# Optimization experiments

Hardware: AMD Instinct MI355X
Metric: run time of the kernel (lower is better)

Reference implementation:

```python
import jax, jax.numpy as jnp
import numpy as np

N_NODES = 50000
N_EDGES = 800000
N_GRAPHS = 64
F_IN, H1, H2, H3, N_CLS = 128, 512, 256, 128, 10
BN_EPS = 1e-5


def setup_inputs() -> dict:
    key = jax.random.key(0)
    ks = jax.random.split(key, 16)

    def lin(k, fi, fo):
        return jax.random.normal(k, (fi, fo), jnp.float32) / np.sqrt(fi).astype(np.float32)

    return {
        "x": jax.random.normal(ks[0], (N_NODES, F_IN), jnp.float32),
        "edge_index": jax.random.randint(ks[1], (2, N_EDGES), 0, N_NODES),
        "batch": jnp.sort(jax.random.randint(ks[2], (N_NODES,), 0, N_GRAPHS)),
        "W1": lin(ks[3], F_IN, H1), "b1": jnp.zeros((H1,), jnp.float32),
        "g1": jnp.ones((H1,), jnp.float32), "be1": jnp.zeros((H1,), jnp.float32),
        "W2": lin(ks[4], H1, H2), "b2": jnp.zeros((H2,), jnp.float32),
        "g2": jnp.ones((H2,), jnp.float32), "be2": jnp.zeros((H2,), jnp.float32),
        "W3": lin(ks[5], H2, H3), "b3": jnp.zeros((H3,), jnp.float32),
        "g3": jnp.ones((H3,), jnp.float32), "be3": jnp.zeros((H3,), jnp.float32),
        "Wo": lin(ks[6], H3, N_CLS), "bo": jnp.zeros((N_CLS,), jnp.float32),
    }


def _gcn_conv(x, row, col, W, b):
    # PyG GCNConv: h = x @ W; add self-loops; sym-normalized scatter-add; + bias
    n = x.shape[0]
    h = x @ W
    loop = jnp.arange(n, dtype=row.dtype)
    row2 = jnp.concatenate([row, loop])  # source nodes
    col2 = jnp.concatenate([col, loop])  # target nodes
    deg = jax.ops.segment_sum(jnp.ones_like(col2, dtype=h.dtype), col2, num_segments=n)
    dinv = jnp.where(deg > 0, jax.lax.rsqrt(deg), 0.0)
    norm = (dinv[row2] * dinv[col2])[:, None]
    agg = jax.ops.segment_sum(h[row2] * norm, col2, num_segments=n)
    return agg + b


def _bn(x, g, b):
    # training-mode BatchNorm over node dim (biased variance, eps=1e-5)
    mean = jnp.mean(x, axis=0)
    var = jnp.mean(jnp.square(x - mean), axis=0)
    return g * (x - mean) * jax.lax.rsqrt(var + BN_EPS) + b


def reference(x, edge_index, batch, W1, b1, g1, be1, W2, b2, g2, be2,
              W3, b3, g3, be3, Wo, bo):
    row, col = edge_index[0], edge_index[1]
    h = jax.nn.relu(_bn(_gcn_conv(x, row, col, W1, b1), g1, be1))
    h = jax.nn.relu(_bn(_gcn_conv(h, row, col, W2, b2), g2, be2))
    h = jax.nn.relu(_bn(_gcn_conv(h, row, col, W3, b3), g3, be3))
    # global_mean_pool over graph ids
    sums = jax.ops.segment_sum(h, batch, num_segments=N_GRAPHS)
    cnt = jax.ops.segment_sum(jnp.ones((h.shape[0],), h.dtype), batch, num_segments=N_GRAPHS)
    pooled = sums / jnp.maximum(cnt, 1.0)[:, None]
    return pooled @ Wo + bo
```

## Files before the change

### kernel.cpp

```cpp
#include <hip/hip_runtime.h>
#include <hip/hip_bf16.h>
#include <cstdint>
#include <cstddef>

#define NNODES 50000
#define NGRAPHS 64

typedef short bf16x8 __attribute__((ext_vector_type(8)));
typedef float f32x4 __attribute__((ext_vector_type(4)));

__device__ inline float bf2f(unsigned short u) {
    return __uint_as_float(((unsigned)u) << 16);
}
__device__ inline unsigned short f2bf(float f) {
    unsigned u = __float_as_uint(f);
    return (unsigned short)((u + 0x7fff + ((u >> 16) & 1)) >> 16);
}
__device__ inline void unpack8(uint4 u, float* v) {
    v[0] = bf2f((unsigned short)(u.x & 0xffff)); v[1] = bf2f((unsigned short)(u.x >> 16));
    v[2] = bf2f((unsigned short)(u.y & 0xffff)); v[3] = bf2f((unsigned short)(u.y >> 16));
    v[4] = bf2f((unsigned short)(u.z & 0xffff)); v[5] = bf2f((unsigned short)(u.z >> 16));
    v[6] = bf2f((unsigned short)(u.w & 0xffff)); v[7] = bf2f((unsigned short)(u.w >> 16));
}

__global__ void deg_count_k(const int* __restrict__ col, int* __restrict__ cnt, int ne) {
    int i = blockIdx.x * blockDim.x + threadIdx.x;
    if (i < ne) atomicAdd(&cnt[col[i]], 1);
}

__global__ __launch_bounds__(256) void scan1_k(const int* __restrict__ cnt, int* __restrict__ offs,
                                               int* __restrict__ bsum, float* __restrict__ dinv, int n) {
    int t = threadIdx.x;
    int base = blockIdx.x * 1024 + t * 4;
    int4 v = {0, 0, 0, 0};
    if (base + 3 < n) v = *reinterpret_cast<const int4*>(cnt + base);
    else {
        if (base + 0 < n) v.x = cnt[base + 0];
        if (base + 1 < n) v.y = cnt[base + 1];
        if (base + 2 < n) v.z = cnt[base + 2];
    }
    if (base + 0 < n) dinv[base + 0] = rsqrtf((float)(v.x + 1));
    if (base + 1 < n) dinv[base + 1] = rsqrtf((float)(v.y + 1));
    if (base + 2 < n) dinv[base + 2] = rsqrtf((float)(v.z + 1));
    if (base + 3 < n) dinv[base + 3] = rsqrtf((float)(v.w + 1));

    int s = v.x + v.y + v.z + v.w;
    __shared__ int lds[256];
    lds[t] = s;
    __syncthreads();
    #pragma unroll
    for (int d = 1; d < 256; d <<= 1) {
        int u = (t >= d) ? lds[t - d] : 0;
        __syncthreads();
        lds[t] += u;
        __syncthreads();
    }
    int excl = lds[t] - s;
    if (t == 255) bsum[blockIdx.x] = lds[t];

    if (base + 3 < n) {
        int4 o;
        o.x = excl; o.y = excl + v.x; o.z = o.y + v.y; o.w = o.z + v.z;
        *reinterpret_cast<int4*>(offs + base) = o;
    } else {
        int e = excl;
        if (base + 0 < n) { offs[base + 0] = e; e += v.x; }
        if (base + 1 < n) { offs[base + 1] = e; e += v.y; }
        if (base + 2 < n) { offs[base + 2] = e; }
    }
}

__global__ __launch_bounds__(256) void scan2_k(int* __restrict__ bsum, int nb) {
    __shared__ int lds[256];
    int t = threadIdx.x;
    int v = (t < nb) ? bsum[t] : 0;
    lds[t] = v;
    __syncthreads();
    #pragma unroll
    for (int d = 1; d < 256; d <<= 1) {
        int u = (t >= d) ? lds[t - d] : 0;
        __syncthreads();
        lds[t] += u;
        __syncthreads();
    }
    if (t < nb) bsum[t] = lds[t] - v;
}

__global__ __launch_bounds__(256) void scan3_k(int* __restrict__ offs, const int* __restrict__ bsum, int n) {
    int base = blockIdx.x * 1024 + threadIdx.x * 4;
    int add = bsum[blockIdx.x];
    if (base + 3 < n) {
        int4 o = *reinterpret_cast<int4*>(offs + base);
        o.x += add; o.y += add; o.z += add; o.w += add;
        *reinterpret_cast<int4*>(offs + base) = o;
    } else {
        for (int k = 0; k < 4; ++k)
            if (base + k < n) offs[base + k] += add;
    }
}

__global__ void scatter_k(const int* __restrict__ row_, const int* __restrict__ col_,
                          const int* __restrict__ offs, int* __restrict__ fill,
                          int* __restrict__ csr_row, int ne) {
    int e = blockIdx.x * blockDim.x + threadIdx.x;
    if (e >= ne) return;
    int r = row_[e], c = col_[e];
    int pos = offs[c] + atomicAdd(&fill[c], 1);
    csr_row[pos] = r;
}

__global__ void cvt_scale_k(const float* __restrict__ in, const float* __restrict__ dinv,
                            unsigned short* __restrict__ out, int n) {
    long long i = (long long)blockIdx.x * blockDim.x + threadIdx.x;
    long long total4 = (long long)n * 32;
    if (i >= total4) return;
    int r = (int)(i >> 5);
    float d = dinv[r];
    float4 v = reinterpret_cast<const float4*>(in)[i];
    uint2 o;
    o.x = (unsigned)f2bf(v.x * d) | ((unsigned)f2bf(v.y * d) << 16);
    o.y = (unsigned)f2bf(v.z * d) | ((unsigned)f2bf(v.w * d) << 16);
    reinterpret_cast<uint2*>(out)[i] = o;
}

__global__ void wtrans_all_k(const float* __restrict__ W1, const float* __restrict__ W2,
                             const float* __restrict__ W3,
                             unsigned short* __restrict__ Wt1, unsigned short* __restrict__ Wt2,
                             unsigned short* __restrict__ Wt3) {
    int idx = blockIdx.x * blockDim.x + threadIdx.x;
    if (idx < 65536) {
        int k = idx >> 9, m = idx & 511;
        Wt1[m * 128 + k] = f2bf(W1[idx]);
    } else if (idx < 196608) {
        int j = idx - 65536;
        int k = j >> 8, m = j & 255;
        Wt2[m * 512 + k] = f2bf(W2[j]);
    } else if (idx < 229376) {
        int j = idx - 196608;
        int k = j >> 7, m = j & 127;
        Wt3[m * 256 + k] = f2bf(W3[j]);
    }
}

template<int FC>
__global__ void agg_s_k(const unsigned short* __restrict__ in, const int* __restrict__ offs,
                        const int* __restrict__ cnt, const int* __restrict__ csr_row,
                        const float* __restrict__ dinv, unsigned short* __restrict__ out, int n) {
    constexpr int F   = 64 * FC;
    constexpr int LPE = (FC == 4) ? 32 : 16;
    constexpr int EPL = 64 / LPE;
    int node = blockIdx.x * 4 + (threadIdx.x >> 6);
    if (node >= n) return;
    int lane = threadIdx.x & 63;
    int sub = lane / LPE;
    int fl  = lane % LPE;
    const size_t foff = (size_t)fl * 8;

    float acc[8] = {};
    if (sub == 0) {
        uint4 u = *reinterpret_cast<const uint4*>(in + (size_t)node * F + foff);
        float v[8]; unpack8(u, v);
        #pragma unroll
        for (int i = 0; i < 8; ++i) acc[i] = v[i];
    }

    int s = offs[node], e1 = s + cnt[node];
    int eb = s;
    for (; eb + 2 * EPL <= e1; eb += 2 * EPL) {
        int r0 = csr_row[eb + sub];
        int r1 = csr_row[eb + EPL + sub];
        uint4 u0 = *reinterpret_cast<const uint4*>(in + (size_t)r0 * F + foff);
        uint4 u1 = *reinterpret_cast<const uint4*>(in + (size_t)r1 * F + foff);
        float v0[8], v1[8];
        unpack8(u0, v0); unpack8(u1, v1);
        #pragma unroll
        for (int i = 0; i < 8; ++i) acc[i] += v0[i] + v1[i];
    }
    for (; eb < e1; eb += EPL) {
        int e = eb + sub;
        bool ok = e < e1;
        int r = csr_row[ok ? e : e1 - 1];
        uint4 u = *reinterpret_cast<const uint4*>(in + (size_t)r * F + foff);
        float v[8]; unpack8(u, v);
        if (ok) {
            #pragma unroll
            for (int i = 0; i < 8; ++i) acc[i] += v[i];
        }
    }

    #pragma unroll
    for (int d = LPE; d < 64; d <<= 1) {
        #pragma unroll
        for (int i = 0; i < 8; ++i) acc[i] += __shfl_xor(acc[i], d, 64);
    }

    if (sub == 0) {
        float dn = dinv[node];
        uint4 o;
        o.x = (unsigned)f2bf(acc[0] * dn) | ((unsigned)f2bf(acc[1] * dn) << 16);
        o.y = (unsigned)f2bf(acc[2] * dn) | ((unsigned)f2bf(acc[3] * dn) << 16);
        o.z = (unsigned)f2bf(acc[4] * dn) | ((unsigned)f2bf(acc[5] * dn) << 16);
        o.w = (unsigned)f2bf(acc[6] * dn) | ((unsigned)f2bf(acc[7] * dn) << 16);
        *reinterpret_cast<uint4*>(out + (size_t)node * F + foff) = o;
    }
}

template<bool BN_A, bool SCALE_OUT, bool STATS>
__global__ __launch_bounds__(256) void gemm_bt_k(const unsigned short* __restrict__ A,
                                                 const unsigned short* __restrict__ B,
                                                 unsigned short* __restrict__ C,
                                                 const float* __restrict__ scale,
                                                 const float* __restrict__ shift,
                                                 const float* __restrict__ dinv,
                                                 float* __restrict__ sums,
                                                 float* __restrict__ sqs,
                                                 int n, int K, int M) {
    __shared__ unsigned short As[128][40];
    __shared__ unsigned short Bs[128][40];
    int tid = threadIdx.x;
    int wid = tid >> 6, lane = tid & 63;
    int wr = wid >> 1, wc = wid & 1;
    int row0 = blockIdx.y * 128, col0 = blockIdx.x * 128;

    f32x4 acc[4][4] = {};

    for (int kt = 0; kt < K; kt += 32) {
        int c8 = (tid & 3) * 8;
        float4 sc0, sc1, sh0, sh1;
        if (BN_A) {
            sc0 = *reinterpret_cast<const float4*>(scale + kt + c8);
            sc1 = *reinterpret_cast<const float4*>(scale + kt + c8 + 4);
            sh0 = *reinterpret_cast<const float4*>(shift + kt + c8);
            sh1 = *reinterpret_cast<const float4*>(shift + kt + c8 + 4);
        }
        #pragma unroll
        for (int h = 0; h < 2; ++h) {
            int r = (tid >> 2) + h * 64;
            int gr = row0 + r;
            bf16x8 va = {};
            if (gr < n) va = *reinterpret_cast<const bf16x8*>(A + (size_t)gr * K + kt + c8);
            if (BN_A) {
                #pragma unroll
                for (int t = 0; t < 8; ++t) {
                    float sct = (t < 4) ? (&sc0.x)[t] : (&sc1.x)[t - 4];
                    float sht = (t < 4) ? (&sh0.x)[t] : (&sh1.x)[t - 4];
                    float f = bf2f((unsigned short)va[t]);
                    va[t] = (short)f2bf(fmaxf(f * sct + sht, 0.f));
                }
            }
            *reinterpret_cast<bf16x8*>(&As[r][c8]) = va;
            bf16x8 vb = *reinterpret_cast<const bf16x8*>(B + (size_t)(col0 + r) * K + kt + c8);
            *reinterpret_cast<bf16x8*>(&Bs[r][c8]) = vb;
        }
        __syncthreads();

        bf16x8 af[4], bfr[4];
        int koff = (lane >> 4) * 8;
        #pragma unroll
        for (int f = 0; f < 4; ++f) {
            af[f]  = *reinterpret_cast<const bf16x8*>(&As[wr * 64 + f * 16 + (lane & 15)][koff]);
            bfr[f] = *reinterpret_cast<const bf16x8*>(&Bs[wc * 64 + f * 16 + (lane & 15)][koff]);
        }
        #pragma unroll
        for (int i = 0; i < 4; ++i)
            #pragma unroll
            for (int j = 0; j < 4; ++j)
                acc[i][j] = __builtin_amdgcn_mfma_f32_16x16x32_bf16(af[i], bfr[j], acc[i][j], 0, 0, 0);
        __syncthreads();
    }

    #pragma unroll
    for (int i = 0; i < 4; ++i) {
        #pragma unroll
        for (int q = 0; q < 4; ++q) {
            int gr = row0 + wr * 64 + i * 16 + (lane >> 4) * 4 + q;
            if (gr < n) {
                float dr = SCALE_OUT ? dinv[gr] : 1.0f;
                #pragma unroll
                for (int j = 0; j < 4; ++j) {
                    int gc = col0 + wc * 64 + j * 16 + (lane & 15);
                    C[(size_t)gr * M + gc] = f2bf(acc[i][j][q] * dr);
                }
            }
        }
    }

    if (STATS) {
        #pragma unroll
        for (int j = 0; j < 4; ++j) {
            float s = 0.f, q = 0.f;
            #pragma unroll
            for (int i = 0; i < 4; ++i)
                #pragma unroll
                for (int p = 0; p < 4; ++p) {
                    float v = acc[i][j][p];
                    s += v; q += v * v;
                }
            s += __shfl_xor(s, 16, 64); s += __shfl_xor(s, 32, 64);
            q += __shfl_xor(q, 16, 64); q += __shfl_xor(q, 32, 64);
            if ((lane >> 4) == 0) {
                int gc = col0 + wc * 64 + j * 16 + (lane & 15);
                atomicAdd(&sums[gc], s);
                atomicAdd(&sqs[gc], q);
            }
        }
    }
}

template<int F>
__global__ __launch_bounds__(256) void bn_stats_k(const unsigned short* __restrict__ in,
                                                  float* __restrict__ stat, int n) {
    constexpr int G   = F / 8;
    constexpr int RPP = 256 / G;
    int g  = threadIdx.x & (G - 1);
    int rl = threadIdx.x / G;

    float s[8] = {}, q[8] = {};
    for (int r = blockIdx.x * RPP + rl; r < n; r += gridDim.x * RPP) {
        uint4 u = *reinterpret_cast<const uint4*>(in + (size_t)r * F + g * 8);
        float v[8]; unpack8(u, v);
        #pragma unroll
        for (int i = 0; i < 8; ++i) { s[i] += v[i]; q[i] += v[i] * v[i]; }
    }

    __shared__ float lds[RPP][F];
    #pragma unroll
    for (int i = 0; i < 8; ++i) lds[rl][g * 8 + i] = s[i];
    __syncthreads();
    if (threadIdx.x < F) {
        float t = 0.f;
        #pragma unroll
        for (int rr = 0; rr < RPP; ++rr) t += lds[rr][threadIdx.x];
        atomicAdd(&stat[threadIdx.x], t);
    }
    __syncthreads();
    #pragma unroll
    for (int i = 0; i < 8; ++i) lds[rl][g * 8 + i] = q[i];
    __syncthreads();
    if (threadIdx.x < F) {
        float t = 0.f;
        #pragma unroll
        for (int rr = 0; rr < RPP; ++rr) t += lds[rr][threadIdx.x];
        atomicAdd(&stat[F + threadIdx.x], t);
    }
}

__global__ void bn_finalize_k(const float* __restrict__ stat,
                              const float* __restrict__ g, const float* __restrict__ be,
                              float* __restrict__ scale, float* __restrict__ shift,
                              int F, float invn) {
    int f = blockIdx.x * blockDim.x + threadIdx.x;
    if (f >= F) return;
    float mean = stat[f] * invn;
    float var  = stat[F + f] * invn - mean * mean;
    float rstd = rsqrtf(var + 1e-5f);
    float sc = g[f] * rstd;
    scale[f] = sc;
    shift[f] = be[f] - mean * sc;
}

__global__ void bounds_k(const int* __restrict__ batch, int* __restrict__ start, int n) {
    int i = blockIdx.x * blockDim.x + threadIdx.x;
    if (i >= n) return;
    int b = batch[i];
    if (i == 0) {
        for (int g = 0; g <= b; ++g) start[g] = 0;
    } else {
        int pb = batch[i - 1];
        for (int g = pb + 1; g <= b; ++g) start[g] = i;
    }
    if (i == n - 1) {
        for (int g = b + 1; g <= NGRAPHS; ++g) start[g] = n;
    }
}

__global__ __launch_bounds__(256) void pool_part_k(const unsigned short* __restrict__ a,
                                                   const int* __restrict__ start,
                                                   const float* __restrict__ scale,
                                                   const float* __restrict__ shift,
                                                   float* __restrict__ partial) {
    int g = blockIdx.x, q = blockIdx.y;
    int s = start[g], e = start[g + 1];
    int nr = e - s;
    int c0 = s + (nr * q) / 4, c1 = s + (nr * (q + 1)) / 4;
    int tf = threadIdx.x & 15, tr = threadIdx.x >> 4;

    float sc[8], sh[8];
    #pragma unroll
    for (int i = 0; i < 8; ++i) { sc[i] = scale[tf * 8 + i]; sh[i] = shift[tf * 8 + i]; }

    float acc[8] = {};
    for (int r = c0 + tr; r < c1; r += 16) {
        uint4 u = *reinterpret_cast<const uint4*>(a + (size_t)r * 128 + tf * 8);
        float v[8]; unpack8(u, v);
        #pragma unroll
        for (int i = 0; i < 8; ++i) acc[i] += fmaxf(v[i] * sc[i] + sh[i], 0.f);
    }

    __shared__ float red[16][128];
    #pragma unroll
    for (int i = 0; i < 8; ++i) red[tr][tf * 8 + i] = acc[i];
    __syncthreads();
    int f = threadIdx.x;
    if (f < 128) {
        float s2 = 0.f;
        #pragma unroll
        for (int t = 0; t < 16; ++t) s2 += red[t][f];
        partial[((size_t)(g * 4 + q)) * 128 + f] = s2;
    }
}

__global__ void final_out_k(const float* __restrict__ partial, const int* __restrict__ start,
                            const float* __restrict__ Wo, const float* __restrict__ bo,
                            float* __restrict__ out) {
    int idx = blockIdx.x * blockDim.x + threadIdx.x;
    if (idx >= NGRAPHS * 10) return;
    int g = idx / 10, c = idx - g * 10;
    float cntf = (float)(start[g + 1] - start[g]);
    float inv = 1.0f / fmaxf(cntf, 1.0f);
    float s = bo[c];
    for (int k = 0; k < 128; ++k) {
        float pk = partial[(size_t)(g * 4 + 0) * 128 + k] + partial[(size_t)(g * 4 + 1) * 128 + k]
                 + partial[(size_t)(g * 4 + 2) * 128 + k] + partial[(size_t)(g * 4 + 3) * 128 + k];
        s += pk * inv * Wo[k * 10 + c];
    }
    out[idx] = s;
}

extern "C" void kernel_launch(void* const* d_in, const int* in_sizes, int n_in,
                              void* d_out, int out_size, void* d_ws, size_t ws_size,
                              hipStream_t stream) {
    const float* x   = (const float*)d_in[0];
    const int*   ei  = (const int*)d_in[1];
    const int*   bat = (const int*)d_in[2];
    const float* W1  = (const float*)d_in[3];
    const float* g1  = (const float*)d_in[5];
    const float* be1 = (const float*)d_in[6];
    const float* W2  = (const float*)d_in[7];
    const float* g2  = (const float*)d_in[9];
    const float* be2 = (const float*)d_in[10];
    const float* W3  = (const float*)d_in[11];
    const float* g3  = (const float*)d_in[13];
    const float* be3 = (const float*)d_in[14];
    const float* Wo  = (const float*)d_in[15];
    const float* bo  = (const float*)d_in[16];
    float* out = (float*)d_out;

    const int n  = in_sizes[2];
    const int ne = in_sizes[1] / 2;
    const int* row = ei;
    const int* col = ei + ne;
    const int NB = (n + 1023) / 1024;

    char* base = (char*)d_ws;
    size_t o = 0;
    auto alloc = [&](size_t bytes) -> char* {
        char* p = base + o;
        o += (bytes + 255) & ~(size_t)255;
        return p;
    };
    int*   cntfill = (int*)alloc((size_t)2 * n * 4);
    int*   cnt  = cntfill;
    int*   fill = cntfill + n;
    float* statall = (float*)alloc((size_t)3 * 1024 * 4);
    float* stat1 = statall;
    float* stat2 = statall + 1024;
    float* stat3 = statall + 2048;
    size_t zspan = (size_t)((char*)(statall + 3 * 1024) - (char*)cntfill);

    int*   offs  = (int*)alloc(n * 4);
    int*   bsum  = (int*)alloc(256 * 4);
    float* dinv  = (float*)alloc(n * 4);
    int*   start = (int*)alloc((NGRAPHS + 1) * 4);
    float* scale = (float*)alloc(512 * 4);
    float* shift = (float*)alloc(512 * 4);
    float* partial = (float*)alloc((size_t)NGRAPHS * 4 * 128 * 4);
    int*   csr_row = (int*)alloc((size_t)ne * 4);
    unsigned short* Wt1 = (unsigned short*)alloc((size_t)128 * 512 * 2);
    unsigned short* Wt2 = (unsigned short*)alloc((size_t)512 * 256 * 2);
    unsigned short* Wt3 = (unsigned short*)alloc((size_t)256 * 128 * 2);
    unsigned short* xs_bf  = (unsigned short*)alloc((size_t)n * 128 * 2);
    unsigned short* ax_bf  = (unsigned short*)alloc((size_t)n * 128 * 2);
    unsigned short* h1_bf  = (unsigned short*)alloc((size_t)n * 512 * 2);
    unsigned short* t2s_bf = (unsigned short*)alloc((size_t)n * 256 * 2);
    unsigned short* a2_bf  = (unsigned short*)alloc((size_t)n * 256 * 2);
    unsigned short* t3s_bf = (unsigned short*)alloc((size_t)n * 128 * 2);
    unsigned short* a3_bf  = (unsigned short*)alloc((size_t)n * 128 * 2);

    hipMemsetAsync(cntfill, 0, zspan, stream);
    deg_count_k<<<(ne + 255) / 256, 256, 0, stream>>>(col, cnt, ne);
    scan1_k<<<NB, 256, 0, stream>>>(cnt, offs, bsum, dinv, n);
    scan2_k<<<1, 256, 0, stream>>>(bsum, NB);
    scan3_k<<<NB, 256, 0, stream>>>(offs, bsum, n);
    scatter_k<<<(ne + 255) / 256, 256, 0, stream>>>(row, col, offs, fill, csr_row, ne);
    bounds_k<<<(n + 255) / 256, 256, 0, stream>>>(bat, start, n);

    cvt_scale_k<<<(unsigned)(((long long)n * 32 + 255) / 256), 256, 0, stream>>>(x, dinv, xs_bf, n);
    wtrans_all_k<<<896, 256, 0, stream>>>(W1, W2, W3, Wt1, Wt2, Wt3);

    agg_s_k<2><<<(n + 3) / 4, 256, 0, stream>>>(xs_bf, offs, cnt, csr_row, dinv, ax_bf, n);
    gemm_bt_k<false, false, true><<<dim3(4, (n + 127) / 128), 256, 0, stream>>>(
        ax_bf, Wt1, h1_bf, nullptr, nullptr, nullptr, stat1, stat1 + 512, n, 128, 512);
    bn_finalize_k<<<2, 256, 0, stream>>>(stat1, g1, be1, scale, shift, 512, 1.0f / n);

    gemm_bt_k<true, true, false><<<dim3(2, (n + 127) / 128), 256, 0, stream>>>(
        h1_bf, Wt2, t2s_bf, scale, shift, dinv, nullptr, nullptr, n, 512, 256);
    agg_s_k<4><<<(n + 3) / 4, 256, 0, stream>>>(t2s_bf, offs, cnt, csr_row, dinv, a2_bf, n);
    bn_stats_k<256><<<1024, 256, 0, stream>>>(a2_bf, stat2, n);
    bn_finalize_k<<<1, 256, 0, stream>>>(stat2, g2, be2, scale, shift, 256, 1.0f / n);

    gemm_bt_k<true, true, false><<<dim3(1, (n + 127) / 128), 256, 0, stream>>>(
        a2_bf, Wt3, t3s_bf, scale, shift, dinv, nullptr, nullptr, n, 256, 128);
    agg_s_k<2><<<(n + 3) / 4, 256, 0, stream>>>(t3s_bf, offs, cnt, csr_row, dinv, a3_bf, n);
    bn_stats_k<128><<<1024, 256, 0, stream>>>(a3_bf, stat3, n);
    bn_finalize_k<<<1, 256, 0, stream>>>(stat3, g3, be3, scale, shift, 128, 1.0f / n);

    pool_part_k<<<dim3(NGRAPHS, 4), 256, 0, stream>>>(a3_bf, start, scale, shift, partial);
    final_out_k<<<3, 256, 0, stream>>>(partial, start, Wo, bo, out);
}
```

Before: 506.2 us.

## Fuse preprocessing, aggregation and tail stages into cooperative persistent kernels

Replaces about twenty small launches with three cooperative kernels that use grid-wide syncs: one for CSR build, conversion and the first aggregation, one for aggregation plus BN stats, and one for aggregation, stats, pooling and output. BN finalize is folded into the GEMM A-load and the pool kernel, so the separate finalize launches go away. The aim is to cut launch overhead and idle gaps between tiny kernels. In exchange, the grid-stride persistent loops can give lower parallelism or occupancy for the gather-heavy aggregation, and grid.sync adds its own cost. A non-cooperative fallback path is kept.

Measured after the change: 2.004 ms. 296% more time.

```diff
diff --git a/kernel.cpp b/kernel.cpp
--- a/kernel.cpp
+++ b/kernel.cpp
@@ -1,9 +1,11 @@
 #include <hip/hip_runtime.h>
 #include <hip/hip_bf16.h>
+#include <hip/hip_cooperative_groups.h>
 #include <cstdint>
 #include <cstddef>
 
-#define NNODES 50000
+namespace cg = cooperative_groups;
+
 #define NGRAPHS 64
 
 typedef short bf16x8 __attribute__((ext_vector_type(8)));
@@ -23,13 +25,10 @@
     v[6] = bf2f((unsigned short)(u.w & 0xffff)); v[7] = bf2f((unsigned short)(u.w >> 16));
 }
 
-__global__ void deg_count_k(const int* __restrict__ col, int* __restrict__ cnt, int ne) {
-    int i = blockIdx.x * blockDim.x + threadIdx.x;
-    if (i < ne) atomicAdd(&cnt[col[i]], 1);
-}
-
-__global__ __launch_bounds__(256) void scan1_k(const int* __restrict__ cnt, int* __restrict__ offs,
-                                               int* __restrict__ bsum, float* __restrict__ dinv, int n) {
+
+__device__ void scan1_body(const int* __restrict__ cnt, int* __restrict__ offs,
+                           int* __restrict__ bsum, float* __restrict__ dinv, int n) {
+    __shared__ int lds1[256];
     int t = threadIdx.x;
     int base = blockIdx.x * 1024 + t * 4;
     int4 v = {0, 0, 0, 0};
@@ -45,18 +44,17 @@
     if (base + 3 < n) dinv[base + 3] = rsqrtf((float)(v.w + 1));
 
     int s = v.x + v.y + v.z + v.w;
-    __shared__ int lds[256];
-    lds[t] = s;
+    lds1[t] = s;
     __syncthreads();
     #pragma unroll
     for (int d = 1; d < 256; d <<= 1) {
-        int u = (t >= d) ? lds[t - d] : 0;
-        __syncthreads();
-        lds[t] += u;
-        __syncthreads();
-    }
-    int excl = lds[t] - s;
-    if (t == 255) bsum[blockIdx.x] = lds[t];
+        int u = (t >= d) ? lds1[t - d] : 0;
+        __syncthreads();
+        lds1[t] += u;
+        __syncthreads();
+    }
+    int excl = lds1[t] - s;
+    if (t == 255) bsum[blockIdx.x] = lds1[t];
 
     if (base + 3 < n) {
         int4 o;
@@ -70,23 +68,23 @@
     }
 }
 
-__global__ __launch_bounds__(256) void scan2_k(int* __restrict__ bsum, int nb) {
-    __shared__ int lds[256];
+__device__ void scan2_body(int* __restrict__ bsum, int nb) {
+    __shared__ int lds2[256];
     int t = threadIdx.x;
     int v = (t < nb) ? bsum[t] : 0;
-    lds[t] = v;
+    lds2[t] = v;
     __syncthreads();
     #pragma unroll
     for (int d = 1; d < 256; d <<= 1) {
-        int u = (t >= d) ? lds[t - d] : 0;
-        __syncthreads();
-        lds[t] += u;
-        __syncthreads();
-    }
-    if (t < nb) bsum[t] = lds[t] - v;
-}
-
-__global__ __launch_bounds__(256) void scan3_k(int* __restrict__ offs, const int* __restrict__ bsum, int n) {
+        int u = (t >= d) ? lds2[t - d] : 0;
+        __syncthreads();
+        lds2[t] += u;
+        __syncthreads();
+    }
+    if (t < nb) bsum[t] = lds2[t] - v;
+}
+
+__device__ void scan3_body(int* __restrict__ offs, const int* __restrict__ bsum, int n) {
     int base = blockIdx.x * 1024 + threadIdx.x * 4;
     int add = bsum[blockIdx.x];
     if (base + 3 < n) {
@@ -99,21 +97,21 @@
     }
 }
 
-__global__ void scatter_k(const int* __restrict__ row_, const int* __restrict__ col_,
-                          const int* __restrict__ offs, int* __restrict__ fill,
-                          int* __restrict__ csr_row, int ne) {
-    int e = blockIdx.x * blockDim.x + threadIdx.x;
-    if (e >= ne) return;
-    int r = row_[e], c = col_[e];
-    int pos = offs[c] + atomicAdd(&fill[c], 1);
-    csr_row[pos] = r;
-}
-
-__global__ void cvt_scale_k(const float* __restrict__ in, const float* __restrict__ dinv,
-                            unsigned short* __restrict__ out, int n) {
-    long long i = (long long)blockIdx.x * blockDim.x + threadIdx.x;
-    long long total4 = (long long)n * 32;
-    if (i >= total4) return;
+__device__ inline void bounds_body(const int* __restrict__ batch, int* __restrict__ start, int i, int n) {
+    int b = batch[i];
+    if (i == 0) {
+        for (int g = 0; g <= b; ++g) start[g] = 0;
+    } else {
+        int pb = batch[i - 1];
+        for (int g = pb + 1; g <= b; ++g) start[g] = i;
+    }
+    if (i == n - 1) {
+        for (int g = b + 1; g <= NGRAPHS; ++g) start[g] = n;
+    }
+}
+
+__device__ inline void cvt_body(const float* __restrict__ in, const float* __restrict__ dinv,
+                                unsigned short* __restrict__ out, long long i) {
     int r = (int)(i >> 5);
     float d = dinv[r];
     float4 v = reinterpret_cast<const float4*>(in)[i];
@@ -123,11 +121,9 @@
     reinterpret_cast<uint2*>(out)[i] = o;
 }
 
-__global__ void wtrans_all_k(const float* __restrict__ W1, const float* __restrict__ W2,
-                             const float* __restrict__ W3,
-                             unsigned short* __restrict__ Wt1, unsigned short* __restrict__ Wt2,
-                             unsigned short* __restrict__ Wt3) {
-    int idx = blockIdx.x * blockDim.x + threadIdx.x;
+__device__ inline void wtrans_body(int idx, const float* __restrict__ W1, const float* __restrict__ W2,
+                                   const float* __restrict__ W3, unsigned short* __restrict__ Wt1,
+                                   unsigned short* __restrict__ Wt2, unsigned short* __restrict__ Wt3) {
     if (idx < 65536) {
         int k = idx >> 9, m = idx & 511;
         Wt1[m * 128 + k] = f2bf(W1[idx]);
@@ -135,7 +131,7 @@
         int j = idx - 65536;
         int k = j >> 8, m = j & 255;
         Wt2[m * 512 + k] = f2bf(W2[j]);
-    } else if (idx < 229376) {
+    } else {
         int j = idx - 196608;
         int k = j >> 7, m = j & 127;
         Wt3[m * 256 + k] = f2bf(W3[j]);
@@ -143,81 +139,271 @@
 }
 
 template<int FC>
-__global__ void agg_s_k(const unsigned short* __restrict__ in, const int* __restrict__ offs,
-                        const int* __restrict__ cnt, const int* __restrict__ csr_row,
-                        const float* __restrict__ dinv, unsigned short* __restrict__ out, int n) {
+__device__ void agg_body(const unsigned short* __restrict__ in, const int* __restrict__ offs,
+                         const int* __restrict__ cnt, const int* __restrict__ csr_row,
+                         const float* __restrict__ dinv, unsigned short* __restrict__ out, int n) {
     constexpr int F   = 64 * FC;
     constexpr int LPE = (FC == 4) ? 32 : 16;
     constexpr int EPL = 64 / LPE;
-    int node = blockIdx.x * 4 + (threadIdx.x >> 6);
-    if (node >= n) return;
+    int wave = threadIdx.x >> 6;
     int lane = threadIdx.x & 63;
     int sub = lane / LPE;
     int fl  = lane % LPE;
     const size_t foff = (size_t)fl * 8;
-
-    float acc[8] = {};
-    if (sub == 0) {
-        uint4 u = *reinterpret_cast<const uint4*>(in + (size_t)node * F + foff);
+    int ngrp = (n + 3) >> 2;
+
+    for (int grp = blockIdx.x; grp < ngrp; grp += gridDim.x) {
+        int node = grp * 4 + wave;
+        if (node >= n) continue;
+
+        float acc[8] = {};
+        if (sub == 0) {
+            uint4 u = *reinterpret_cast<const uint4*>(in + (size_t)node * F + foff);
+            float v[8]; unpack8(u, v);
+            #pragma unroll
+            for (int i = 0; i < 8; ++i) acc[i] = v[i];
+        }
+
+        int s = offs[node], e1 = s + cnt[node];
+        int eb = s;
+        for (; eb + 2 * EPL <= e1; eb += 2 * EPL) {
+            int r0 = csr_row[eb + sub];
+            int r1 = csr_row[eb + EPL + sub];
+            uint4 u0 = *reinterpret_cast<const uint4*>(in + (size_t)r0 * F + foff);
+            uint4 u1 = *reinterpret_cast<const uint4*>(in + (size_t)r1 * F + foff);
+            float v0[8], v1[8];
+            unpack8(u0, v0); unpack8(u1, v1);
+            #pragma unroll
+            for (int i = 0; i < 8; ++i) acc[i] += v0[i] + v1[i];
+        }
+        for (; eb < e1; eb += EPL) {
+            int e = eb + sub;
+            bool ok = e < e1;
+            int r = csr_row[ok ? e : e1 - 1];
+            uint4 u = *reinterpret_cast<const uint4*>(in + (size_t)r * F + foff);
+            float v[8]; unpack8(u, v);
+            if (ok) {
+                #pragma unroll
+                for (int i = 0; i < 8; ++i) acc[i] += v[i];
+            }
+        }
+
+        #pragma unroll
+        for (int d = LPE; d < 64; d <<= 1) {
+            #pragma unroll
+            for (int i = 0; i < 8; ++i) acc[i] += __shfl_xor(acc[i], d, 64);
+        }
+
+        if (sub == 0) {
+            float dn = dinv[node];
+            uint4 o;
+            o.x = (unsigned)f2bf(acc[0] * dn) | ((unsigned)f2bf(acc[1] * dn) << 16);
+            o.y = (unsigned)f2bf(acc[2] * dn) | ((unsigned)f2bf(acc[3] * dn) << 16);
+            o.z = (unsigned)f2bf(acc[4] * dn) | ((unsigned)f2bf(acc[5] * dn) << 16);
+            o.w = (unsigned)f2bf(acc[6] * dn) | ((unsigned)f2bf(acc[7] * dn) << 16);
+            *reinterpret_cast<uint4*>(out + (size_t)node * F + foff) = o;
+        }
+    }
+}
+
+template<int F>
+__device__ void bn_stats_body(const unsigned short* __restrict__ in, float* __restrict__ stat, int n) {
+    constexpr int G   = F / 8;
+    constexpr int RPP = 256 / G;
+    int g  = threadIdx.x & (G - 1);
+    int rl = threadIdx.x / G;
+
+    float s[8] = {}, q[8] = {};
+    for (int r = blockIdx.x * RPP + rl; r < n; r += gridDim.x * RPP) {
+        uint4 u = *reinterpret_cast<const uint4*>(in + (size_t)r * F + g * 8);
         float v[8]; unpack8(u, v);
         #pragma unroll
-        for (int i = 0; i < 8; ++i) acc[i] = v[i];
-    }
-
-    int s = offs[node], e1 = s + cnt[node];
-    int eb = s;
-    for (; eb + 2 * EPL <= e1; eb += 2 * EPL) {
-        int r0 = csr_row[eb + sub];
-        int r1 = csr_row[eb + EPL + sub];
-        uint4 u0 = *reinterpret_cast<const uint4*>(in + (size_t)r0 * F + foff);
-        uint4 u1 = *reinterpret_cast<const uint4*>(in + (size_t)r1 * F + foff);
-        float v0[8], v1[8];
-        unpack8(u0, v0); unpack8(u1, v1);
-        #pragma unroll
-        for (int i = 0; i < 8; ++i) acc[i] += v0[i] + v1[i];
-    }
-    for (; eb < e1; eb += EPL) {
-        int e = eb + sub;
-        bool ok = e < e1;
-        int r = csr_row[ok ? e : e1 - 1];
-        uint4 u = *reinterpret_cast<const uint4*>(in + (size_t)r * F + foff);
-        float v[8]; unpack8(u, v);
-        if (ok) {
+        for (int i = 0; i < 8; ++i) { s[i] += v[i]; q[i] += v[i] * v[i]; }
+    }
+
+    __shared__ float ldsb[RPP][F];
+    #pragma unroll
+    for (int i = 0; i < 8; ++i) ldsb[rl][g * 8 + i] = s[i];
+    __syncthreads();
+    if (threadIdx.x < F) {
+        float t = 0.f;
+        #pragma unroll
+        for (int rr = 0; rr < RPP; ++rr) t += ldsb[rr][threadIdx.x];
+        atomicAdd(&stat[threadIdx.x], t);
+    }
+    __syncthreads();
+    #pragma unroll
+    for (int i = 0; i < 8; ++i) ldsb[rl][g * 8 + i] = q[i];
+    __syncthreads();
+    if (threadIdx.x < F) {
+        float t = 0.f;
+        #pragma unroll
+        for (int rr = 0; rr < RPP; ++rr) t += ldsb[rr][threadIdx.x];
+        atomicAdd(&stat[F + threadIdx.x], t);
+    }
+}
+
+__device__ void pool_body(const unsigned short* __restrict__ a, const int* __restrict__ start,
+                          const float* __restrict__ stat3, const float* __restrict__ g3,
+                          const float* __restrict__ be3, float invn, float* __restrict__ partial) {
+    __shared__ float scp[128], shp[128];
+    __shared__ float red[16][128];
+    int tid = threadIdx.x;
+    if (tid < 128) {
+        float mean = stat3[tid] * invn;
+        float var  = stat3[128 + tid] * invn - mean * mean;
+        float sc = g3[tid] * rsqrtf(var + 1e-5f);
+        scp[tid] = sc;
+        shp[tid] = be3[tid] - mean * sc;
+    }
+    __syncthreads();
+    int tf = tid & 15, tr = tid >> 4;
+    float sc[8], sh[8];
+    #pragma unroll
+    for (int i = 0; i < 8; ++i) { sc[i] = scp[tf * 8 + i]; sh[i] = shp[tf * 8 + i]; }
+
+    for (int job = blockIdx.x; job < NGRAPHS * 4; job += gridDim.x) {
+        int g = job >> 2, q = job & 3;
+        int s = start[g], e = start[g + 1];
+        int nr = e - s;
+        int c0 = s + (nr * q) / 4, c1 = s + (nr * (q + 1)) / 4;
+
+        float acc[8] = {};
+        for (int r = c0 + tr; r < c1; r += 16) {
+            uint4 u = *reinterpret_cast<const uint4*>(a + (size_t)r * 128 + tf * 8);
+            float v[8]; unpack8(u, v);
             #pragma unroll
-            for (int i = 0; i < 8; ++i) acc[i] += v[i];
-        }
-    }
-
-    #pragma unroll
-    for (int d = LPE; d < 64; d <<= 1) {
-        #pragma unroll
-        for (int i = 0; i < 8; ++i) acc[i] += __shfl_xor(acc[i], d, 64);
-    }
-
-    if (sub == 0) {
-        float dn = dinv[node];
-        uint4 o;
-        o.x = (unsigned)f2bf(acc[0] * dn) | ((unsigned)f2bf(acc[1] * dn) << 16);
-        o.y = (unsigned)f2bf(acc[2] * dn) | ((unsigned)f2bf(acc[3] * dn) << 16);
-        o.z = (unsigned)f2bf(acc[4] * dn) | ((unsigned)f2bf(acc[5] * dn) << 16);
-        o.w = (unsigned)f2bf(acc[6] * dn) | ((unsigned)f2bf(acc[7] * dn) << 16);
-        *reinterpret_cast<uint4*>(out + (size_t)node * F + foff) = o;
-    }
-}
-
-template<bool BN_A, bool SCALE_OUT, bool STATS>
+            for (int i = 0; i < 8; ++i) acc[i] += fmaxf(v[i] * sc[i] + sh[i], 0.f);
+        }
+        #pragma unroll
+        for (int i = 0; i < 8; ++i) red[tr][tf * 8 + i] = acc[i];
+        __syncthreads();
+        if (tid < 128) {
+            float s2 = 0.f;
+            #pragma unroll
+            for (int t = 0; t < 16; ++t) s2 += red[t][tid];
+            partial[((size_t)job) * 128 + tid] = s2;
+        }
+        __syncthreads();
+    }
+}
+
+__device__ void final_body(const float* __restrict__ partial, const int* __restrict__ start,
+                           const float* __restrict__ Wo, const float* __restrict__ bo,
+                           float* __restrict__ out, int gtid, int gsz) {
+    for (int idx = gtid; idx < NGRAPHS * 10; idx += gsz) {
+        int g = idx / 10, c = idx - g * 10;
+        float cntf = (float)(start[g + 1] - start[g]);
+        float inv = 1.0f / fmaxf(cntf, 1.0f);
+        float s = bo[c];
+        for (int k = 0; k < 128; ++k) {
+            float pk = partial[(size_t)(g * 4 + 0) * 128 + k] + partial[(size_t)(g * 4 + 1) * 128 + k]
+                     + partial[(size_t)(g * 4 + 2) * 128 + k] + partial[(size_t)(g * 4 + 3) * 128 + k];
+            s += pk * inv * Wo[k * 10 + c];
+        }
+        out[idx] = s;
+    }
+}
+
+
+struct PrepArgs {
+    const float* x; const int* row; const int* col; const int* bat;
+    const float* W1; const float* W2; const float* W3;
+    int* cnt; int* fill; float* statall; int* offs; int* bsum; float* dinv; int* start;
+    int* csr_row;
+    unsigned short* Wt1; unsigned short* Wt2; unsigned short* Wt3;
+    unsigned short* xs; unsigned short* ax;
+    int n; int ne; int nb;
+};
+
+__global__ __launch_bounds__(256) void prep_coop_k(PrepArgs a) {
+    cg::grid_group grid = cg::this_grid();
+    int gsz  = gridDim.x * 256;
+    int gtid = blockIdx.x * 256 + threadIdx.x;
+
+    for (int i = gtid; i < a.n; i += gsz) { a.cnt[i] = 0; a.fill[i] = 0; }
+    for (int i = gtid; i < 3 * 1024; i += gsz) a.statall[i] = 0.f;
+    grid.sync();
+    for (int e = gtid; e < a.ne; e += gsz) atomicAdd(&a.cnt[a.col[e]], 1);
+    grid.sync();
+    if (blockIdx.x < a.nb) scan1_body(a.cnt, a.offs, a.bsum, a.dinv, a.n);
+    grid.sync();
+    if (blockIdx.x == 0) scan2_body(a.bsum, a.nb);
+    grid.sync();
+    if (blockIdx.x < a.nb) scan3_body(a.offs, a.bsum, a.n);
+    grid.sync();
+    for (int e = gtid; e < a.ne; e += gsz) {
+        int r = a.row[e], c = a.col[e];
+        int pos = a.offs[c] + atomicAdd(&a.fill[c], 1);
+        a.csr_row[pos] = r;
+    }
+    for (int i = gtid; i < a.n; i += gsz) bounds_body(a.bat, a.start, i, a.n);
+    long long total4 = (long long)a.n * 32;
+    for (long long i = gtid; i < total4; i += gsz) cvt_body(a.x, a.dinv, a.xs, i);
+    for (int i = gtid; i < 229376; i += gsz) wtrans_body(i, a.W1, a.W2, a.W3, a.Wt1, a.Wt2, a.Wt3);
+    grid.sync();
+    agg_body<2>(a.xs, a.offs, a.cnt, a.csr_row, a.dinv, a.ax, a.n);
+}
+
+struct MidArgs {
+    const unsigned short* t2s; const int* offs; const int* cnt; const int* csr_row;
+    const float* dinv; unsigned short* a2; float* stat2; int n;
+};
+
+__global__ __launch_bounds__(256) void mid_coop_k(MidArgs a) {
+    cg::grid_group grid = cg::this_grid();
+    agg_body<4>(a.t2s, a.offs, a.cnt, a.csr_row, a.dinv, a.a2, a.n);
+    grid.sync();
+    bn_stats_body<256>(a.a2, a.stat2, a.n);
+}
+
+struct TailArgs {
+    const unsigned short* t3s; const int* offs; const int* cnt; const int* csr_row;
+    const float* dinv; unsigned short* a3; float* stat3;
+    const float* g3; const float* be3; const int* start;
+    const float* Wo; const float* bo; float* partial; float* out; int n;
+};
+
+__global__ __launch_bounds__(256) void tail_coop_k(TailArgs a) {
+    cg::grid_group grid = cg::this_grid();
+    agg_body<2>(a.t3s, a.offs, a.cnt, a.csr_row, a.dinv, a.a3, a.n);
+    grid.sync();
+    bn_stats_body<128>(a.a3, a.stat3, a.n);
+    grid.sync();
+    pool_body(a.a3, a.start, a.stat3, a.g3, a.be3, 1.0f / a.n, a.partial);
+    grid.sync();
+    final_body(a.partial, a.start, a.Wo, a.bo, a.out, blockIdx.x * 256 + threadIdx.x, gridDim.x * 256);
+}
+
+template<bool BN_STAT, bool SCALE_OUT, bool STATS>
 __global__ __launch_bounds__(256) void gemm_bt_k(const unsigned short* __restrict__ A,
                                                  const unsigned short* __restrict__ B,
                                                  unsigned short* __restrict__ C,
-                                                 const float* __restrict__ scale,
-                                                 const float* __restrict__ shift,
+                                                 const float* __restrict__ stat_in,
+                                                 const float* __restrict__ gamma,
+                                                 const float* __restrict__ beta,
+                                                 float invn,
                                                  const float* __restrict__ dinv,
                                                  float* __restrict__ sums,
                                                  float* __restrict__ sqs,
                                                  int n, int K, int M) {
     __shared__ unsigned short As[128][40];
     __shared__ unsigned short Bs[128][40];
+    __shared__ float scs[BN_STAT ? 512 : 1];
+    __shared__ float shs[BN_STAT ? 512 : 1];
     int tid = threadIdx.x;
+
+    if (BN_STAT) {
+        for (int f = tid; f < K; f += 256) {
+            float mean = stat_in[f] * invn;
+            float var  = stat_in[K + f] * invn - mean * mean;
+            float sc = gamma[f] * rsqrtf(var + 1e-5f);
+            scs[f] = sc;
+            shs[f] = beta[f] - mean * sc;
+        }
+        __syncthreads();
+    }
+
     int wid = tid >> 6, lane = tid & 63;
     int wr = wid >> 1, wc = wid & 1;
     int row0 = blockIdx.y * 128, col0 = blockIdx.x * 128;
@@ -227,11 +413,11 @@
     for (int kt = 0; kt < K; kt += 32) {
         int c8 = (tid & 3) * 8;
         float4 sc0, sc1, sh0, sh1;
-        if (BN_A) {
-            sc0 = *reinterpret_cast<const float4*>(scale + kt + c8);
-            sc1 = *reinterpret_cast<const float4*>(scale + kt + c8 + 4);
-            sh0 = *reinterpret_cast<const float4*>(shift + kt + c8);
-            sh1 = *reinterpret_cast<const float4*>(shift + kt + c8 + 4);
+        if (BN_STAT) {
+            sc0 = *reinterpret_cast<const float4*>(&scs[kt + c8]);
+            sc1 = *reinterpret_cast<const float4*>(&scs[kt + c8 + 4]);
+            sh0 = *reinterpret_cast<const float4*>(&shs[kt + c8]);
+            sh1 = *reinterpret_cast<const float4*>(&shs[kt + c8 + 4]);
         }
         #pragma unroll
         for (int h = 0; h < 2; ++h) {
@@ -239,7 +425,7 @@
             int gr = row0 + r;
             bf16x8 va = {};
             if (gr < n) va = *reinterpret_cast<const bf16x8*>(A + (size_t)gr * K + kt + c8);
-            if (BN_A) {
+            if (BN_STAT) {
                 #pragma unroll
                 for (int t = 0; t < 8; ++t) {
                     float sct = (t < 4) ? (&sc0.x)[t] : (&sc1.x)[t - 4];
@@ -307,125 +493,58 @@
     }
 }
 
+
+__global__ void deg_count_k(const int* __restrict__ col, int* __restrict__ cnt, int ne) {
+    int i = blockIdx.x * blockDim.x + threadIdx.x;
+    if (i < ne) atomicAdd(&cnt[col[i]], 1);
+}
+__global__ __launch_bounds__(256) void scan1_k(const int* cnt, int* offs, int* bsum, float* dinv, int n) {
+    scan1_body(cnt, offs, bsum, dinv, n);
+}
+__global__ __launch_bounds__(256) void scan2_k(int* bsum, int nb) { scan2_body(bsum, nb); }
+__global__ __launch_bounds__(256) void scan3_k(int* offs, const int* bsum, int n) { scan3_body(offs, bsum, n); }
+
+__global__ void prep3_k(const int* __restrict__ row_, const int* __restrict__ col_,
+                        const int* __restrict__ offs, int* __restrict__ fill, int* __restrict__ csr_row,
+                        const int* __restrict__ bat, int* __restrict__ start,
+                        const float* __restrict__ x, const float* __restrict__ dinv,
+                        unsigned short* __restrict__ xs,
+                        const float* __restrict__ W1, const float* __restrict__ W2, const float* __restrict__ W3,
+                        unsigned short* __restrict__ Wt1, unsigned short* __restrict__ Wt2,
+                        unsigned short* __restrict__ Wt3, int n, int ne) {
+    int gsz  = gridDim.x * blockDim.x;
+    int gtid = blockIdx.x * blockDim.x + threadIdx.x;
+    for (int e = gtid; e < ne; e += gsz) {
+        int r = row_[e], c = col_[e];
+        int pos = offs[c] + atomicAdd(&fill[c], 1);
+        csr_row[pos] = r;
+    }
+    for (int i = gtid; i < n; i += gsz) bounds_body(bat, start, i, n);
+    long long total4 = (long long)n * 32;
+    for (long long i = gtid; i < total4; i += gsz) cvt_body(x, dinv, xs, i);
+    for (int i = gtid; i < 229376; i += gsz) wtrans_body(i, W1, W2, W3, Wt1, Wt2, Wt3);
+}
+
+template<int FC>
+__global__ void agg_k(const unsigned short* in, const int* offs, const int* cnt, const int* csr_row,
+                      const float* dinv, unsigned short* out, int n) {
+    agg_body<FC>(in, offs, cnt, csr_row, dinv, out, n);
+}
 template<int F>
-__global__ __launch_bounds__(256) void bn_stats_k(const unsigned short* __restrict__ in,
-                                                  float* __restrict__ stat, int n) {
-    constexpr int G   = F / 8;
-    constexpr int RPP = 256 / G;
-    int g  = threadIdx.x & (G - 1);
-    int rl = threadIdx.x / G;
-
-    float s[8] = {}, q[8] = {};
-    for (int r = blockIdx.x * RPP + rl; r < n; r += gridDim.x * RPP) {
-        uint4 u = *reinterpret_cast<const uint4*>(in + (size_t)r * F + g * 8);
-        float v[8]; unpack8(u, v);
-        #pragma unroll
-        for (int i = 0; i < 8; ++i) { s[i] += v[i]; q[i] += v[i] * v[i]; }
-    }
-
-    __shared__ float lds[RPP][F];
-    #pragma unroll
-    for (int i = 0; i < 8; ++i) lds[rl][g * 8 + i] = s[i];
-    __syncthreads();
-    if (threadIdx.x < F) {
-        float t = 0.f;
-        #pragma unroll
-        for (int rr = 0; rr < RPP; ++rr) t += lds[rr][threadIdx.x];
-        atomicAdd(&stat[threadIdx.x], t);
-    }
-    __syncthreads();
-    #pragma unroll
-    for (int i = 0; i < 8; ++i) lds[rl][g * 8 + i] = q[i];
-    __syncthreads();
-    if (threadIdx.x < F) {
-        float t = 0.f;
-        #pragma unroll
-        for (int rr = 0; rr < RPP; ++rr) t += lds[rr][threadIdx.x];
-        atomicAdd(&stat[F + threadIdx.x], t);
-    }
-}
-
-__global__ void bn_finalize_k(const float* __restrict__ stat,
-                              const float* __restrict__ g, const float* __restrict__ be,
-                              float* __restrict__ scale, float* __restrict__ shift,
-                              int F, float invn) {
-    int f = blockIdx.x * blockDim.x + threadIdx.x;
-    if (f >= F) return;
-    float mean = stat[f] * invn;
-    float var  = stat[F + f] * invn - mean * mean;
-    float rstd = rsqrtf(var + 1e-5f);
-    float sc = g[f] * rstd;
-    scale[f] = sc;
-    shift[f] = be[f] - mean * sc;
-}
-
-__global__ void bounds_k(const int* __restrict__ batch, int* __restrict__ start, int n) {
-    int i = blockIdx.x * blockDim.x + threadIdx.x;
-    if (i >= n) return;
-    int b = batch[i];
-    if (i == 0) {
-        for (int g = 0; g <= b; ++g) start[g] = 0;
-    } else {
-        int pb = batch[i - 1];
-        for (int g = pb + 1; g <= b; ++g) start[g] = i;
-    }
-    if (i == n - 1) {
-        for (int g = b + 1; g <= NGRAPHS; ++g) start[g] = n;
-    }
-}
-
-__global__ __launch_bounds__(256) void pool_part_k(const unsigned short* __restrict__ a,
-                                                   const int* __restrict__ start,
-                                                   const float* __restrict__ scale,
-                                                   const float* __restrict__ shift,
-                                                   float* __restrict__ partial) {
-    int g = blockIdx.x, q = blockIdx.y;
-    int s = start[g], e = start[g + 1];
-    int nr = e - s;
-    int c0 = s + (nr * q) / 4, c1 = s + (nr * (q + 1)) / 4;
-    int tf = threadIdx.x & 15, tr = threadIdx.x >> 4;
-
-    float sc[8], sh[8];
-    #pragma unroll
-    for (int i = 0; i < 8; ++i) { sc[i] = scale[tf * 8 + i]; sh[i] = shift[tf * 8 + i]; }
-
-    float acc[8] = {};
-    for (int r = c0 + tr; r < c1; r += 16) {
-        uint4 u = *reinterpret_cast<const uint4*>(a + (size_t)r * 128 + tf * 8);
-        float v[8]; unpack8(u, v);
-        #pragma unroll
-        for (int i = 0; i < 8; ++i) acc[i] += fmaxf(v[i] * sc[i] + sh[i], 0.f);
-    }
-
-    __shared__ float red[16][128];
-    #pragma unroll
-    for (int i = 0; i < 8; ++i) red[tr][tf * 8 + i] = acc[i];
-    __syncthreads();
-    int f = threadIdx.x;
-    if (f < 128) {
-        float s2 = 0.f;
-        #pragma unroll
-        for (int t = 0; t < 16; ++t) s2 += red[t][f];
-        partial[((size_t)(g * 4 + q)) * 128 + f] = s2;
-    }
-}
-
-__global__ void final_out_k(const float* __restrict__ partial, const int* __restrict__ start,
-                            const float* __restrict__ Wo, const float* __restrict__ bo,
-                            float* __restrict__ out) {
-    int idx = blockIdx.x * blockDim.x + threadIdx.x;
-    if (idx >= NGRAPHS * 10) return;
-    int g = idx / 10, c = idx - g * 10;
-    float cntf = (float)(start[g + 1] - start[g]);
-    float inv = 1.0f / fmaxf(cntf, 1.0f);
-    float s = bo[c];
-    for (int k = 0; k < 128; ++k) {
-        float pk = partial[(size_t)(g * 4 + 0) * 128 + k] + partial[(size_t)(g * 4 + 1) * 128 + k]
-                 + partial[(size_t)(g * 4 + 2) * 128 + k] + partial[(size_t)(g * 4 + 3) * 128 + k];
-        s += pk * inv * Wo[k * 10 + c];
-    }
-    out[idx] = s;
-}
+__global__ __launch_bounds__(256) void bn_stats_k(const unsigned short* in, float* stat, int n) {
+    bn_stats_body<F>(in, stat, n);
+}
+__global__ __launch_bounds__(256) void pool_k(const unsigned short* a, const int* start,
+                                              const float* stat3, const float* g3, const float* be3,
+                                              float invn, float* partial) {
+    pool_body(a, start, stat3, g3, be3, invn, partial);
+}
+__global__ void final_out_k(const float* partial, const int* start, const float* Wo,
+                            const float* bo, float* out) {
+    final_body(partial, start, Wo, bo, out, blockIdx.x * blockDim.x + threadIdx.x,
+               gridDim.x * blockDim.x);
+}
+
 
 extern "C" void kernel_launch(void* const* d_in, const int* in_sizes, int n_in,
                               void* d_out, int out_size, void* d_ws, size_t ws_size,
@@ -466,14 +585,11 @@
     float* stat1 = statall;
     float* stat2 = statall + 1024;
     float* stat3 = statall + 2048;
-    size_t zspan = (size_t)((char*)(statall + 3 * 1024) - (char*)cntfill);
 
     int*   offs  = (int*)alloc(n * 4);
     int*   bsum  = (int*)alloc(256 * 4);
     float* dinv  = (float*)alloc(n * 4);
     int*   start = (int*)alloc((NGRAPHS + 1) * 4);
-    float* scale = (float*)alloc(512 * 4);
-    float* shift = (float*)alloc(512 * 4);
     float* partial = (float*)alloc((size_t)NGRAPHS * 4 * 128 * 4);
     int*   csr_row = (int*)alloc((size_t)ne * 4);
     unsigned short* Wt1 = (unsigned short*)alloc((size_t)128 * 512 * 2);
@@ -487,34 +603,72 @@
     unsigned short* t3s_bf = (unsigned short*)alloc((size_t)n * 128 * 2);
     unsigned short* a3_bf  = (unsigned short*)alloc((size_t)n * 128 * 2);
 
-    hipMemsetAsync(cntfill, 0, zspan, stream);
-    deg_count_k<<<(ne + 255) / 256, 256, 0, stream>>>(col, cnt, ne);
-    scan1_k<<<NB, 256, 0, stream>>>(cnt, offs, bsum, dinv, n);
-    scan2_k<<<1, 256, 0, stream>>>(bsum, NB);
-    scan3_k<<<NB, 256, 0, stream>>>(offs, bsum, n);
-    scatter_k<<<(ne + 255) / 256, 256, 0, stream>>>(row, col, offs, fill, csr_row, ne);
-    bounds_k<<<(n + 255) / 256, 256, 0, stream>>>(bat, start, n);
-
-    cvt_scale_k<<<(unsigned)(((long long)n * 32 + 255) / 256), 256, 0, stream>>>(x, dinv, xs_bf, n);
-    wtrans_all_k<<<896, 256, 0, stream>>>(W1, W2, W3, Wt1, Wt2, Wt3);
-
-    agg_s_k<2><<<(n + 3) / 4, 256, 0, stream>>>(xs_bf, offs, cnt, csr_row, dinv, ax_bf, n);
+    const float invn = 1.0f / (float)n;
+
+    PrepArgs pa = { x, row, col, bat, W1, W2, W3, cnt, fill, statall, offs, bsum, dinv, start,
+                    csr_row, Wt1, Wt2, Wt3, xs_bf, ax_bf, n, ne, NB };
+    MidArgs  ma = { t2s_bf, offs, cnt, csr_row, dinv, a2_bf, stat2, n };
+    TailArgs ta = { t3s_bf, offs, cnt, csr_row, dinv, a3_bf, stat3, g3, be3, start,
+                    Wo, bo, partial, out, n };
+
+    bool coop = true;
+    {
+        int occ = 0;
+        if (hipOccupancyMaxActiveBlocksPerMultiprocessor(&occ, prep_coop_k, 256, 0) != hipSuccess || occ < 1)
+            occ = 2;
+        int G = occ * 256; if (G > 4096) G = 4096;
+        void* args[] = { &pa };
+        hipError_t e = hipLaunchCooperativeKernel((const void*)prep_coop_k, dim3(G), dim3(256), args, 0, stream);
+        if (e != hipSuccess) { coop = false; (void)hipGetLastError(); }
+    }
+    if (!coop) {
+        hipMemsetAsync(cntfill, 0, (size_t)2 * n * 4, stream);
+        hipMemsetAsync(statall, 0, 3 * 1024 * 4, stream);
+        deg_count_k<<<(ne + 255) / 256, 256, 0, stream>>>(col, cnt, ne);
+        scan1_k<<<NB, 256, 0, stream>>>(cnt, offs, bsum, dinv, n);
+        scan2_k<<<1, 256, 0, stream>>>(bsum, NB);
+        scan3_k<<<NB, 256, 0, stream>>>(offs, bsum, n);
+        prep3_k<<<2048, 256, 0, stream>>>(row, col, offs, fill, csr_row, bat, start,
+                                          x, dinv, xs_bf, W1, W2, W3, Wt1, Wt2, Wt3, n, ne);
+        agg_k<2><<<(n + 3) / 4, 256, 0, stream>>>(xs_bf, offs, cnt, csr_row, dinv, ax_bf, n);
+    }
+
     gemm_bt_k<false, false, true><<<dim3(4, (n + 127) / 128), 256, 0, stream>>>(
-        ax_bf, Wt1, h1_bf, nullptr, nullptr, nullptr, stat1, stat1 + 512, n, 128, 512);
-    bn_finalize_k<<<2, 256, 0, stream>>>(stat1, g1, be1, scale, shift, 512, 1.0f / n);
+        ax_bf, Wt1, h1_bf, nullptr, nullptr, nullptr, 0.f, nullptr, stat1, stat1 + 512, n, 128, 512);
 
     gemm_bt_k<true, true, false><<<dim3(2, (n + 127) / 128), 256, 0, stream>>>(
-        h1_bf, Wt2, t2s_bf, scale, shift, dinv, nullptr, nullptr, n, 512, 256);
-    agg_s_k<4><<<(n + 3) / 4, 256, 0, stream>>>(t2s_bf, offs, cnt, csr_row, dinv, a2_bf, n);
-    bn_stats_k<256><<<1024, 256, 0, stream>>>(a2_bf, stat2, n);
-    bn_finalize_k<<<1, 256, 0, stream>>>(stat2, g2, be2, scale, shift, 256, 1.0f / n);
+        h1_bf, Wt2, t2s_bf, stat1, g1, be1, invn, dinv, nullptr, nullptr, n, 512, 256);
+
+    if (coop) {
+        int occ = 0;
+        if (hipOccupancyMaxActiveBlocksPerMultiprocessor(&occ, mid_coop_k, 256, 0) != hipSuccess || occ < 1)
+            occ = 2;
+        int G = occ * 256; if (G > 4096) G = 4096;
+        void* args[] = { &ma };
+        hipError_t e = hipLaunchCooperativeKernel((const void*)mid_coop_k, dim3(G), dim3(256), args, 0, stream);
+        if (e != hipSuccess) { coop = false; (void)hipGetLastError(); }
+    }
+    if (!coop) {
+        agg_k<4><<<(n + 3) / 4, 256, 0, stream>>>(t2s_bf, offs, cnt, csr_row, dinv, a2_bf, n);
+        bn_stats_k<256><<<1024, 256, 0, stream>>>(a2_bf, stat2, n);
+    }
 
     gemm_bt_k<true, true, false><<<dim3(1, (n + 127) / 128), 256, 0, stream>>>(
-        a2_bf, Wt3, t3s_bf, scale, shift, dinv, nullptr, nullptr, n, 256, 128);
-    agg_s_k<2><<<(n + 3) / 4, 256, 0, stream>>>(t3s_bf, offs, cnt, csr_row, dinv, a3_bf, n);
-    bn_stats_k<128><<<1024, 256, 0, stream>>>(a3_bf, stat3, n);
-    bn_finalize_k<<<1, 256, 0, stream>>>(stat3, g3, be3, scale, shift, 128, 1.0f / n);
-
-    pool_part_k<<<dim3(NGRAPHS, 4), 256, 0, stream>>>(a3_bf, start, scale, shift, partial);
-    final_out_k<<<3, 256, 0, stream>>>(partial, start, Wo, bo, out);
-}
+        a2_bf, Wt3, t3s_bf, stat2, g2, be2, invn, dinv, nullptr, nullptr, n, 256, 128);
+
+    if (coop) {
+        int occ = 0;
+        if (hipOccupancyMaxActiveBlocksPerMultiprocessor(&occ, tail_coop_k, 256, 0) != hipSuccess || occ < 1)
+            occ = 2;
+        int G = occ * 256; if (G > 4096) G = 4096;
+        void* args[] = { &ta };
+        hipError_t e = hipLaunchCooperativeKernel((const void*)tail_coop_k, dim3(G), dim3(256), args, 0, stream);
+        if (e != hipSuccess) { coop = false; (void)hipGetLastError(); }
+    }
+    if (!coop) {
+        agg_k<2><<<(n + 3) / 4, 256, 0, stream>>>(t3s_bf, offs, cnt, csr_row, dinv, a3_bf, n);
+        bn_stats_k<128><<<1024, 256, 0, stream>>>(a3_bf, stat3, n);
+        pool_k<<<256, 256, 0, stream>>>(a3_bf, start, stat3, g3, be3, invn, partial);
+        final_out_k<<<3, 256, 0, stream>>>(partial, start, Wo, bo, out);
+    }
+}
```
